# Optimization experiments

Measured on AMD Instinct MI355X. Metric: run time of the kernel, lower is better.

## Reference

```python
import jax, jax.numpy as jnp
import numpy as np

B, S, D_MODEL, N_HEADS, D_FF = 4, 2048, 1024, 16, 4096
HEAD_DIM = D_MODEL // N_HEADS
NUM_BUCKETS, MAX_DISTANCE = 32, 128
EPS = 1e-6


def _relative_position_bucket(relative_position, num_buckets=NUM_BUCKETS, max_distance=MAX_DISTANCE):
    # bidirectional (encoder) variant, matching T5RelativePositionBias
    n = -relative_position
    nb = num_buckets // 2
    ret = (n < 0).astype(jnp.int32) * nb
    n = jnp.abs(n)
    max_exact = nb // 2
    val_if_large = max_exact + (
        jnp.log(jnp.maximum(n, 1).astype(jnp.float32) / max_exact)
        / np.log(max_distance / max_exact) * (nb - max_exact)
    ).astype(jnp.int32)
    val_if_large = jnp.minimum(val_if_large, nb - 1)
    return ret + jnp.where(n < max_exact, n, val_if_large)


def t5_position_bias(rel_emb, q_len, k_len):
    ctx = jnp.arange(q_len)[:, None]
    mem = jnp.arange(k_len)[None, :]
    rp_bucket = _relative_position_bucket(mem - ctx)          # [S, S]
    bias = rel_emb[rp_bucket]                                  # [S, S, H]
    return jnp.transpose(bias, (2, 0, 1))[None]                # [1, H, S, S]


def layer_norm(x, g, b):
    mu = jnp.mean(x, axis=-1, keepdims=True)
    var = jnp.mean(jnp.square(x - mu), axis=-1, keepdims=True)
    return (x - mu) * jax.lax.rsqrt(var + EPS) * g + b


def setup_inputs() -> dict:
    key = jax.random.key(0)
    ks = jax.random.split(key, 20)
    s = 0.02
    p = {
        'src': jax.random.normal(ks[0], (B, S, D_MODEL), jnp.float32),
        'wq': jax.random.normal(ks[1], (D_MODEL, D_MODEL), jnp.float32) * s,
        'bq': jnp.zeros((D_MODEL,), jnp.float32),
        'wk': jax.random.normal(ks[2], (D_MODEL, D_MODEL), jnp.float32) * s,
        'bk': jnp.zeros((D_MODEL,), jnp.float32),
        'wv': jax.random.normal(ks[3], (D_MODEL, D_MODEL), jnp.float32) * s,
        'bv': jnp.zeros((D_MODEL,), jnp.float32),
        'wo': jax.random.normal(ks[4], (D_MODEL, D_MODEL), jnp.float32) * s,
        'bo': jnp.zeros((D_MODEL,), jnp.float32),
        'w1': jax.random.normal(ks[5], (D_MODEL, D_FF), jnp.float32) * s,
        'b1': jnp.zeros((D_FF,), jnp.float32),
        'w2': jax.random.normal(ks[6], (D_FF, D_MODEL), jnp.float32) * s,
        'b2': jnp.zeros((D_MODEL,), jnp.float32),
        'ln1_g': jnp.ones((D_MODEL,), jnp.float32),
        'ln1_b': jnp.zeros((D_MODEL,), jnp.float32),
        'ln2_g': jnp.ones((D_MODEL,), jnp.float32),
        'ln2_b': jnp.zeros((D_MODEL,), jnp.float32),
        'rel_emb': jax.random.normal(ks[7], (NUM_BUCKETS, N_HEADS), jnp.float32) * s,
    }
    return p


def reference(src, wq, bq, wk, bk, wv, bv, wo, bo, w1, b1, w2, b2,
              ln1_g, ln1_b, ln2_g, ln2_b, rel_emb):
    b, s, _ = src.shape

    # --- self-attention block (pre-norm) ---
    xn = layer_norm(src, ln1_g, ln1_b)
    q = (xn @ wq + bq).reshape(b, s, N_HEADS, HEAD_DIM).transpose(0, 2, 1, 3)
    k = (xn @ wk + bk).reshape(b, s, N_HEADS, HEAD_DIM).transpose(0, 2, 1, 3)
    v = (xn @ wv + bv).reshape(b, s, N_HEADS, HEAD_DIM).transpose(0, 2, 1, 3)

    bias = t5_position_bias(rel_emb, s, s)                       # [1,H,S,S]
    scores = jnp.einsum('bhqd,bhkd->bhqk', q, k) / np.sqrt(HEAD_DIM) + bias
    attn = jax.nn.softmax(scores, axis=-1)
    ctx = jnp.einsum('bhqk,bhkd->bhqd', attn, v)                 # [B,H,S,Dh]
    ctx = ctx.transpose(0, 2, 1, 3).reshape(b, s, D_MODEL)
    x = src + (ctx @ wo + bo)

    # --- FFN block (pre-norm, ReLU) ---
    yn = layer_norm(x, ln2_g, ln2_b)
    y = jax.nn.relu(yn @ w1 + b1) @ w2 + b2
    return x + y
```

## Files before the change

### kernel.cpp

```cpp
#include <hip/hip_runtime.h>
#include <math.h>

typedef unsigned short u16;

#define S_LEN 2048
#define BSZ 4
#define DM 1024
#define NH 16
#define HD 64
#define DFF 4096
#define ROWS (BSZ * S_LEN)
#define LOG2E 1.4426950408889634f

typedef __attribute__((__ext_vector_type__(8))) __bf16 bf16x8;
typedef __attribute__((__ext_vector_type__(8))) short short8;
typedef __attribute__((__ext_vector_type__(4))) short short4v;
typedef __attribute__((__ext_vector_type__(4))) float f32x4;
typedef __attribute__((__ext_vector_type__(4))) float float4v;

__device__ __forceinline__ float bf2f(u16 u) {
    union { unsigned int i; float f; } c; c.i = ((unsigned int)u) << 16; return c.f;
}
__device__ __forceinline__ u16 f2bf(float f) {
    union { float f; unsigned int i; } c; c.f = f;
    unsigned int r = c.i + 0x7fffu + ((c.i >> 16) & 1u);
    return (u16)(r >> 16);
}
__device__ __forceinline__ u16 f2bf_cvt(float f) {
    __bf16 h = (__bf16)f;
    return __builtin_bit_cast(u16, h);
}
__device__ __forceinline__ float ldin(const void* p, long i, int f32) {
    return f32 ? ((const float*)p)[i] : bf2f(((const u16*)p)[i]);
}
__device__ __forceinline__ int dtype_f32(const u16* ln1g) {
    return ln1g[0] != 0x3F80;
}
__device__ __forceinline__ void gl_lds16(const void* g, void* l) {
    __builtin_amdgcn_global_load_lds(
        (const __attribute__((address_space(1))) unsigned int*)g,
        (__attribute__((address_space(3))) unsigned int*)l, 16, 0, 0);
}

#define BARR  asm volatile("s_barrier" ::: "memory")
#define LGKM0 asm volatile("s_waitcnt lgkmcnt(0)" ::: "memory")
#define VM4   asm volatile("s_waitcnt vmcnt(4)" ::: "memory")
#define VM0   asm volatile("s_waitcnt vmcnt(0)" ::: "memory")

__device__ __forceinline__ void tr_tile(
    const void* __restrict__ src, u16* __restrict__ dst, int N, int K,
    int bx, int by, int f32, int tid, u16 (*t)[72])
{
#pragma unroll
    for (int i = 0; i < 2; i++) {
        int c = tid + i * 256;
        int row = c >> 3, col = (c & 7) * 8;
        long off = (long)(by * 64 + row) * N + bx * 64 + col;
        short8 v;
        if (f32) {
            const float* s = (const float*)src + off;
            float4v a = *(const float4v*)s;
            float4v b = *(const float4v*)(s + 4);
#pragma unroll
            for (int k = 0; k < 4; k++) { v[k] = (short)f2bf(a[k]); v[k + 4] = (short)f2bf(b[k]); }
        } else {
            v = *(const short8*)((const u16*)src + off);
        }
        *(short8*)(&t[row][col]) = v;
    }
    __syncthreads();
#pragma unroll
    for (int i = 0; i < 2; i++) {
        int c = tid + i * 256;
        int row = c >> 3, col = (c & 7) * 8;
        short8 v;
#pragma unroll
        for (int jj = 0; jj < 8; jj++) v[jj] = (short)t[col + jj][row];
        *(short8*)(dst + (long)(bx * 64 + row) * K + by * 64 + col) = v;
    }
}

__global__ __launch_bounds__(256) void transpose4(
    const void* wq, const void* wk, const void* wv, const void* wo,
    u16* __restrict__ wqkvt, u16* __restrict__ wot, const u16* __restrict__ ln1g)
{
    __shared__ u16 t[64][72];
    int z = blockIdx.z;
    const void* src = (z == 0) ? wq : (z == 1) ? wk : (z == 2) ? wv : wo;
    u16* dst = (z < 3) ? wqkvt + (long)z * 1024 * 1024 : wot;
    tr_tile(src, dst, DM, DM, blockIdx.x, blockIdx.y, dtype_f32(ln1g), threadIdx.x, t);
}

__global__ __launch_bounds__(256) void transpose2(
    const void* w1, const void* w2, u16* __restrict__ w1t, u16* __restrict__ w2t,
    const u16* __restrict__ ln1g)
{
    __shared__ u16 t[64][72];
    int f32 = dtype_f32(ln1g);
    if (blockIdx.z == 0)
        tr_tile(w1, w1t, DFF, DM, blockIdx.x, blockIdx.y, f32, threadIdx.x, t);
    else
        tr_tile(w2, w2t, DM, DFF, blockIdx.y, blockIdx.x, f32, threadIdx.x, t);
}

__global__ __launch_bounds__(256) void vtrans(
    const u16* __restrict__ v, u16* __restrict__ vt)
{
    __shared__ u16 t[64][72];
    int s0 = blockIdx.x * 64;
    int bh = blockIdx.y;
    const u16* src = v + (long)bh * S_LEN * HD;
    u16* dst = vt + (long)bh * HD * S_LEN;
    int tid = threadIdx.x;
#pragma unroll
    for (int i = 0; i < 2; i++) {
        int c = tid + i * 256;
        int row = c >> 3, col = (c & 7) * 8;
        *(short8*)(&t[row][col]) = *(const short8*)(src + (long)(s0 + row) * HD + col);
    }
    __syncthreads();
#pragma unroll
    for (int i = 0; i < 2; i++) {
        int c = tid + i * 256;
        int row = c >> 3, col = (c & 7) * 8;
        short8 o;
#pragma unroll
        for (int jj = 0; jj < 8; jj++) o[jj] = (short)t[col + jj][row];
        *(short8*)(dst + (long)row * S_LEN + s0 + col) = o;
    }
}

__global__ __launch_bounds__(256) void prep_kernel(
    const void* bq, const void* bk, const void* bv, const void* bo,
    const void* b1, const void* b2, const void* l1g, const void* l1b,
    const void* l2g, const void* l2b, const void* rel,
    u16* __restrict__ smalls, float* __restrict__ bias_full)
{
    int f32 = dtype_f32((const u16*)l1g);
    int tid = blockIdx.x * blockDim.x + threadIdx.x;
    if (tid < 13312) {
        float v;
        if      (tid < 1024)  v = ldin(bq,  tid,         f32);
        else if (tid < 2048)  v = ldin(bk,  tid - 1024,  f32);
        else if (tid < 3072)  v = ldin(bv,  tid - 2048,  f32);
        else if (tid < 4096)  v = ldin(bo,  tid - 3072,  f32);
        else if (tid < 8192)  v = ldin(b1,  tid - 4096,  f32);
        else if (tid < 9216)  v = ldin(b2,  tid - 8192,  f32);
        else if (tid < 10240) v = ldin(l1g, tid - 9216,  f32);
        else if (tid < 11264) v = ldin(l1b, tid - 10240, f32);
        else if (tid < 12288) v = ldin(l2g, tid - 11264, f32);
        else                  v = ldin(l2b, tid - 12288, f32);
        smalls[tid] = f2bf(v);
    }
    if (tid < 4095 * 16) {
        int dIdx = tid >> 4;
        int h = tid & 15;
        int delta = dIdx - 2047;
        int n = -delta;
        int ret = (n < 0) ? 16 : 0;
        int na = (n < 0) ? -n : n;
        int bkt;
        if (na < 8) {
            bkt = na;
        } else {
            float tval = logf((float)na * 0.125f) * 2.8853900817779268f;
            int v = 8 + (int)tval;
            bkt = v < 15 ? v : 15;
        }
        bkt += ret;
        bias_full[h * 4095 + dIdx] = ldin(rel, bkt * 16 + h, f32) * LOG2E;
    }
}

__global__ __launch_bounds__(256) void ln_kernel(
    const void* __restrict__ xin, int external, const u16* __restrict__ ln1g,
    const u16* __restrict__ g, const u16* __restrict__ bta, u16* __restrict__ out)
{
    int f32 = external ? dtype_f32(ln1g) : 0;
    int row = blockIdx.x;
    int tid = threadIdx.x;
    float vals[4];
    if (f32) {
        float4v v = *(const float4v*)((const float*)xin + (long)row * DM + tid * 4);
#pragma unroll
        for (int k = 0; k < 4; k++) vals[k] = v[k];
    } else {
        short4v v = *(const short4v*)((const u16*)xin + (long)row * DM + tid * 4);
#pragma unroll
        for (int k = 0; k < 4; k++) vals[k] = bf2f((u16)v[k]);
    }
    float s1 = 0.f, s2 = 0.f;
#pragma unroll
    for (int k = 0; k < 4; k++) { s1 += vals[k]; s2 += vals[k] * vals[k]; }
#pragma unroll
    for (int off = 32; off > 0; off >>= 1) {
        s1 += __shfl_xor(s1, off);
        s2 += __shfl_xor(s2, off);
    }
    __shared__ float ps1[4], ps2[4];
    int wave = tid >> 6, lane = tid & 63;
    if (lane == 0) { ps1[wave] = s1; ps2[wave] = s2; }
    __syncthreads();
    s1 = ps1[0] + ps1[1] + ps1[2] + ps1[3];
    s2 = ps2[0] + ps2[1] + ps2[2] + ps2[3];
    float mu = s1 * (1.0f / DM);
    float var = s2 * (1.0f / DM) - mu * mu;
    float rs = rsqrtf(var + 1e-6f);
    short4v ov;
#pragma unroll
    for (int k = 0; k < 4; k++) {
        float gv = bf2f(g[tid * 4 + k]);
        float bv = bf2f(bta[tid * 4 + k]);
        ov[k] = (short)f2bf((vals[k] - mu) * rs * gv + bv);
    }
    *(short4v*)(out + (long)row * DM + tid * 4) = ov;
}

#define BM 128
#define BN 128
#define BK 64

__global__ __launch_bounds__(256, 3) void gemm_bt(
    const u16* __restrict__ A, const u16* __restrict__ Bt,
    const u16* __restrict__ bias, int M, int N, int K, int mode,
    u16* __restrict__ out_q, u16* __restrict__ out_k, u16* __restrict__ out_v,
    const void* __restrict__ res, void* __restrict__ outp,
    const u16* __restrict__ ln1g)
{
    __shared__ u16 As[BM][BK];
    __shared__ u16 Bs[BN][BK];
    int tid = threadIdx.x;
    int wave = tid >> 6, lane = tid & 63;
    int quad = lane >> 4, l16 = lane & 15;
    int wr = (wave >> 1) * 64, wc = (wave & 1) * 64;

    int nwg = gridDim.x * gridDim.y;
    int bid = blockIdx.y * gridDim.x + blockIdx.x;
    int chunk = nwg >> 3;
    int swz = (bid & 7) * chunk + (bid >> 3);
    int bx = swz % gridDim.x, by = swz / gridDim.x;

    long m0 = (long)by * BM, n0 = (long)bx * BN;
    int flg = (mode == 2 || mode == 4) ? dtype_f32(ln1g) : 0;

    int prow = tid >> 3;
    int pchk = tid & 7;
    int cchk = pchk ^ (prow & 7);
    int skc = cchk * 8;
    int pkc = pchk * 8;
    int rxor = l16 & 7;

    f32x4 acc[4][4];
    f32x4 z = {0.f, 0.f, 0.f, 0.f};
#pragma unroll
    for (int i = 0; i < 4; i++)
#pragma unroll
        for (int j = 0; j < 4; j++) acc[i][j] = z;

    for (int k0 = 0; k0 < K; k0 += BK) {
        __syncthreads();
#pragma unroll
        for (int ro = 0; ro < 4; ro++) {
            gl_lds16(A  + (m0 + ro * 32 + prow) * K + k0 + skc, &As[ro * 32 + prow][pkc]);
            gl_lds16(Bt + (n0 + ro * 32 + prow) * K + k0 + skc, &Bs[ro * 32 + prow][pkc]);
        }
        __syncthreads();
#pragma unroll
        for (int t = 0; t < 2; t++) {
            int rc = ((t * 4 + quad) ^ rxor) * 8;
            bf16x8 af[4], bfr[4];
#pragma unroll
            for (int i = 0; i < 4; i++)
                af[i] = __builtin_bit_cast(bf16x8, *(const short8*)(&As[wr + i * 16 + l16][rc]));
#pragma unroll
            for (int j = 0; j < 4; j++)
                bfr[j] = __builtin_bit_cast(bf16x8, *(const short8*)(&Bs[wc + j * 16 + l16][rc]));
#pragma unroll
            for (int i = 0; i < 4; i++)
#pragma unroll
                for (int j = 0; j < 4; j++)
                    acc[i][j] = __builtin_amdgcn_mfma_f32_16x16x32_bf16(af[i], bfr[j], acc[i][j], 0, 0, 0);
        }
    }

#pragma unroll
    for (int i = 0; i < 4; i++) {
#pragma unroll
        for (int j = 0; j < 4; j++) {
#pragma unroll
            for (int r = 0; r < 4; r++) {
                long gr = m0 + wr + i * 16 + quad * 4 + r;
                long gc = n0 + wc + j * 16 + l16;
                float val = acc[i][j][r] + bf2f(bias[gc]);
                if (mode == 1) {
                    int sel = (int)(gc >> 10);
                    int cc = (int)(gc & 1023);
                    int h = cc >> 6, d = cc & 63;
                    int b = (int)(gr >> 11), s = (int)(gr & 2047);
                    u16* dst = (sel == 0) ? out_q : (sel == 1 ? out_k : out_v);
                    dst[(((long)(b * NH + h)) * S_LEN + s) * HD + d] = f2bf(val);
                } else if (mode == 2) {
                    long idx = gr * N + gc;
                    float rv = flg ? ((const float*)res)[idx]
                                   : bf2f(((const u16*)res)[idx]);
                    ((u16*)outp)[idx] = f2bf(val + rv);
                } else if (mode == 3) {
                    ((u16*)outp)[gr * N + gc] = f2bf(val > 0.f ? val : 0.f);
                } else {
                    long idx = gr * N + gc;
                    float o = val + bf2f(((const u16*)res)[idx]);
                    if (flg) ((float*)outp)[idx] = o;
                    else     ((u16*)outp)[idx]  = f2bf(o);
                }
            }
        }
    }
}

#define TM 256
#define TN 256
#define TK 64

#define PHASE(bi, q, STAGE, WAITV)                                             \
    {                                                                          \
        if ((q) == 0) {                                                        \
            _Pragma("unroll")                                                  \
            for (int j = 0; j < 4; j++) {                                      \
                _Pragma("unroll")                                              \
                for (int t = 0; t < 2; t++)                                    \
                    bfr[j][t] = __builtin_bit_cast(bf16x8, *(const short8*)(   \
                        &Bs[bi][wn * 64 + j * 16 + l16][((t * 4 + quad) ^ rxor) * 8])); \
            }                                                                  \
        }                                                                      \
        _Pragma("unroll")                                                      \
        for (int i = 0; i < 2; i++) {                                          \
            _Pragma("unroll")                                                  \
            for (int t = 0; t < 2; t++)                                        \
                af[i][t] = __builtin_bit_cast(bf16x8, *(const short8*)(        \
                    &As[bi][wm * 128 + ((q) * 2 + i) * 16 + l16][((t * 4 + quad) ^ rxor) * 8])); \
        }                                                                      \
        STAGE                                                                  \
        WAITV;                                                                 \
        BARR;                                                                  \
        LGKM0;                                                                 \
        __builtin_amdgcn_sched_barrier(0);                                     \
        __builtin_amdgcn_s_setprio(1);                                         \
        _Pragma("unroll")                                                      \
        for (int i = 0; i < 2; i++) {                                          \
            _Pragma("unroll")                                                  \
            for (int j = 0; j < 4; j++) {                                      \
                acc[(q) * 2 + i][j] = __builtin_amdgcn_mfma_f32_16x16x32_bf16( \
                    af[i][0], bfr[j][0], acc[(q) * 2 + i][j], 0, 0, 0);        \
                acc[(q) * 2 + i][j] = __builtin_amdgcn_mfma_f32_16x16x32_bf16( \
                    af[i][1], bfr[j][1], acc[(q) * 2 + i][j], 0, 0, 0);        \
            }                                                                  \
        }                                                                      \
        __builtin_amdgcn_s_setprio(0);                                         \
        BARR;                                                                  \
    }

__global__ __launch_bounds__(512, 2) void gemm256(
    const u16* __restrict__ A, const u16* __restrict__ Bt,
    const u16* __restrict__ bias, int M, int N, int K, int mode,
    u16* __restrict__ out_q, u16* __restrict__ out_k, u16* __restrict__ out_v,
    u16* __restrict__ outp)
{
    __shared__ u16 As[2][TM][TK];
    __shared__ u16 Bs[2][TN][TK];

    int tid = threadIdx.x;
    int wavei = tid >> 6, lane = tid & 63;
    int quad = lane >> 4, l16 = lane & 15;
    int wm = wavei >> 2, wn = wavei & 3;

    int nwg = gridDim.x * gridDim.y;
    int bid = blockIdx.y * gridDim.x + blockIdx.x;
    int chunk = nwg >> 3;
    int swz = (bid & 7) * chunk + (bid >> 3);
    int bx = swz % gridDim.x, by = swz / gridDim.x;
    long m0 = (long)by * TM, n0 = (long)bx * TN;

    int srow = tid >> 3;
    int pchk = tid & 7;
    int cchk = pchk ^ (srow & 7);
    int rxor = l16 & 7;

    int NT = K / TK;

    auto stageA = [&](int bufi, int h, int t) {
        const u16* g = A + (m0 + h * 128 + srow) * (long)K + (long)t * TK + cchk * 8;
        gl_lds16(g,                 &As[bufi][h * 128 + srow     ][pchk * 8]);
        gl_lds16(g + 64 * (long)K,  &As[bufi][h * 128 + srow + 64][pchk * 8]);
    };
    auto stageB = [&](int bufi, int h, int t) {
        const u16* g = Bt + (n0 + h * 128 + srow) * (long)K + (long)t * TK + cchk * 8;
        gl_lds16(g,                 &Bs[bufi][h * 128 + srow     ][pchk * 8]);
        gl_lds16(g + 64 * (long)K,  &Bs[bufi][h * 128 + srow + 64][pchk * 8]);
    };

    f32x4 acc[8][4];
    f32x4 z = {0.f, 0.f, 0.f, 0.f};
#pragma unroll
    for (int i = 0; i < 8; i++)
#pragma unroll
        for (int j = 0; j < 4; j++) acc[i][j] = z;

    bf16x8 bfr[4][2];
    bf16x8 af[2][2];

    stageA(0, 0, 0); stageA(0, 1, 0); stageB(0, 0, 0); stageB(0, 1, 0);
    stageB(1, 0, 1); stageB(1, 1, 1);
    VM4;
    BARR;

    for (int kt = 0; kt < NT - 2; kt += 2) {
        PHASE(0, 0, { stageA(1, 0, kt + 1); stageA(1, 1, kt + 1); }, (void)0);
        PHASE(0, 1, { stageB(0, 0, kt + 2); }, (void)0);
        PHASE(0, 2, { stageB(0, 1, kt + 2); }, (void)0);
        PHASE(0, 3, {}, VM4);
        PHASE(1, 0, { stageA(0, 0, kt + 2); }, (void)0);
        PHASE(1, 1, { stageA(0, 1, kt + 2); stageB(1, 0, kt + 3); }, (void)0);
        PHASE(1, 2, { stageB(1, 1, kt + 3); }, (void)0);
        PHASE(1, 3, {}, VM4);
    }
    PHASE(0, 0, { stageA(1, 0, NT - 1); stageA(1, 1, NT - 1); }, (void)0);
    PHASE(0, 1, {}, (void)0);
    PHASE(0, 2, {}, (void)0);
    PHASE(0, 3, {}, VM0);
    PHASE(1, 0, {}, (void)0);
    PHASE(1, 1, {}, (void)0);
    PHASE(1, 2, {}, (void)0);
    PHASE(1, 3, {}, (void)0);

#pragma unroll
    for (int i = 0; i < 8; i++) {
#pragma unroll
        for (int j = 0; j < 4; j++) {
#pragma unroll
            for (int r = 0; r < 4; r++) {
                long gr = m0 + wm * 128 + i * 16 + quad * 4 + r;
                long gc = n0 + wn * 64 + j * 16 + l16;
                float val = acc[i][j][r] + bf2f(bias[gc]);
                if (mode == 1) {
                    int sel = (int)(gc >> 10);
                    int cc = (int)(gc & 1023);
                    int h = cc >> 6, d = cc & 63;
                    int b = (int)(gr >> 11), s = (int)(gr & 2047);
                    u16* dst = (sel == 0) ? out_q : (sel == 1 ? out_k : out_v);
                    dst[(((long)(b * NH + h)) * S_LEN + s) * HD + d] = f2bf(val);
                } else {
                    outp[gr * (long)N + gc] = f2bf(val > 0.f ? val : 0.f);
                }
            }
        }
    }
}

__global__ __launch_bounds__(256, 4) void attn_kernel(
    const u16* __restrict__ Qg, const u16* __restrict__ Kg, const u16* __restrict__ Vtg,
    const float* __restrict__ bias_full, u16* __restrict__ ctx)
{
    __shared__ u16 Ks[64][64];
    __shared__ u16 Vt[64][64];
    __shared__ u16 Ps[64][72];
    __shared__ u16 bias_s[2112];

    int bh = blockIdx.y;
    int b = bh >> 4, h = bh & 15;
    int q0 = blockIdx.x * 64;
    const u16* Q  = Qg  + (long)bh * S_LEN * HD;
    const u16* Kp = Kg  + (long)bh * S_LEN * HD;
    const u16* Vp = Vtg + (long)bh * HD * S_LEN;

    int tid = threadIdx.x;
    int wave = tid >> 6, lane = tid & 63;
    int quad = lane >> 4, l16 = lane & 15;

    for (int i = tid; i < 2112; i += 256)
        bias_s[i] = f2bf(bias_full[h * 4095 + 1984 + i - q0]);
    float Bneg = bias_full[h * 4095 + 0];
    float Bpos = bias_full[h * 4095 + 4094];

    int prow = tid >> 3, pchk = tid & 7;
    int cchk = pchk ^ (prow & 7);
    int rxor = l16 & 7;
    int rc0 = (quad ^ rxor) * 8;
    int rc1 = ((4 + quad) ^ rxor) * 8;

    bf16x8 aq[2];
#pragma unroll
    for (int t = 0; t < 2; t++)
        aq[t] = __builtin_bit_cast(bf16x8,
            *(const short8*)(Q + (long)(q0 + wave * 16 + l16) * HD + t * 32 + quad * 8));

    bf16x8 ones;
#pragma unroll
    for (int i = 0; i < 8; i++) ones[i] = (__bf16)1.0f;

    f32x4 o[4];
    f32x4 z = {0.f, 0.f, 0.f, 0.f};
#pragma unroll
    for (int j = 0; j < 4; j++) o[j] = z;
    f32x4 lacc = z;

    int ib = 63 + quad * 4 - wave * 16 - l16;
    const float c0 = 0.125f * LOG2E;

    for (int t0 = 0; t0 < S_LEN; t0 += 64) {
        __syncthreads();
#pragma unroll
        for (int ro = 0; ro < 2; ro++) {
            gl_lds16(Kp + (long)(t0 + ro * 32 + prow) * HD + cchk * 8,
                     &Ks[ro * 32 + prow][pchk * 8]);
            gl_lds16(Vp + (long)(ro * 32 + prow) * S_LEN + t0 + cchk * 8,
                     &Vt[ro * 32 + prow][pchk * 8]);
        }
        __syncthreads();

        f32x4 s_[4];
#pragma unroll
        for (int j = 0; j < 4; j++) {
            f32x4 a = z;
            bf16x8 kf0 = __builtin_bit_cast(bf16x8, *(const short8*)(&Ks[j * 16 + l16][rc0]));
            a = __builtin_amdgcn_mfma_f32_16x16x32_bf16(kf0, aq[0], a, 0, 0, 0);
            bf16x8 kf1 = __builtin_bit_cast(bf16x8, *(const short8*)(&Ks[j * 16 + l16][rc1]));
            a = __builtin_amdgcn_mfma_f32_16x16x32_bf16(kf1, aq[1], a, 0, 0, 0);
            s_[j] = a;
        }
        int d0 = t0 - q0;
        int nearb = (d0 >= -153 && d0 <= 153);
        float bconst = (d0 > 0) ? Bpos : Bneg;
#pragma unroll
        for (int j = 0; j < 4; j++) {
            short4v pk;
#pragma unroll
            for (int r = 0; r < 4; r++) {
                float bl = nearb ? bf2f(bias_s[ib + t0 + j * 16 + r]) : bconst;
                float p = __builtin_amdgcn_exp2f(fminf(fmaf(s_[j][r], c0, bl), 100.0f));
                pk[r] = (short)f2bf_cvt(p);
            }
            *(short4v*)(&Ps[wave * 16 + l16][j * 16 + quad * 4]) = pk;
        }

        bf16x8 ap[2];
#pragma unroll
        for (int tt = 0; tt < 2; tt++)
            ap[tt] = __builtin_bit_cast(bf16x8,
                *(const short8*)(&Ps[wave * 16 + l16][tt * 32 + quad * 8]));
        lacc = __builtin_amdgcn_mfma_f32_16x16x32_bf16(ap[0], ones, lacc, 0, 0, 0);
        lacc = __builtin_amdgcn_mfma_f32_16x16x32_bf16(ap[1], ones, lacc, 0, 0, 0);
#pragma unroll
        for (int j = 0; j < 4; j++) {
            f32x4 t = o[j];
            bf16x8 bv0 = __builtin_bit_cast(bf16x8, *(const short8*)(&Vt[j * 16 + l16][rc0]));
            t = __builtin_amdgcn_mfma_f32_16x16x32_bf16(ap[0], bv0, t, 0, 0, 0);
            bf16x8 bv1 = __builtin_bit_cast(bf16x8, *(const short8*)(&Vt[j * 16 + l16][rc1]));
            t = __builtin_amdgcn_mfma_f32_16x16x32_bf16(ap[1], bv1, t, 0, 0, 0);
            o[j] = t;
        }
    }

#pragma unroll
    for (int r = 0; r < 4; r++) {
        int qr = wave * 16 + quad * 4 + r;
        float linv = 1.0f / lacc[r];
        long srow = (long)(b * S_LEN + q0 + qr);
#pragma unroll
        for (int j = 0; j < 4; j++)
            ctx[srow * DM + h * HD + j * 16 + l16] = f2bf(o[j][r] * linv);
    }
}

extern "C" void kernel_launch(void* const* d_in, const int* in_sizes, int n_in,
                              void* d_out, int out_size, void* d_ws, size_t ws_size,
                              hipStream_t stream)
{
    const void* src  = d_in[0];
    const void* wq   = d_in[1];
    const void* bq   = d_in[2];
    const void* wk   = d_in[3];
    const void* bk   = d_in[4];
    const void* wv   = d_in[5];
    const void* bv   = d_in[6];
    const void* wo   = d_in[7];
    const void* bo   = d_in[8];
    const void* w1   = d_in[9];
    const void* b1   = d_in[10];
    const void* w2   = d_in[11];
    const void* b2   = d_in[12];
    const void* ln1g = d_in[13];
    const void* ln1b = d_in[14];
    const void* ln2g = d_in[15];
    const void* ln2b = d_in[16];
    const void* rel  = d_in[17];
    const u16* l1g16 = (const u16*)ln1g;

    char* ws = (char*)d_ws;
    const long MB = 1L << 20;
    u16*   smalls = (u16*)  (ws);
    float* bfull  = (float*)(ws + 65536);
    u16*   xn     = (u16*)  (ws + 1  * MB);
    u16*   vtg    = (u16*)  (ws + 1  * MB);
    u16*   qws    = (u16*)  (ws + 17 * MB);
    u16*   kws    = (u16*)  (ws + 33 * MB);
    u16*   vws    = (u16*)  (ws + 49 * MB);
    u16*   hbuf   = (u16*)  (ws + 1  * MB);
    u16*   ctx    = (u16*)  (ws + 65 * MB);
    u16*   yn     = (u16*)  (ws + 65 * MB);
    u16*   xbf    = (u16*)  (ws + 81 * MB);
    u16*   wqkvt  = (u16*)  (ws + 97 * MB);
    u16*   wot    = (u16*)  (ws + 103 * MB);
    u16*   w1t    = (u16*)  (ws + 97 * MB);
    u16*   w2t    = (u16*)  (ws + 105 * MB);

    transpose4<<<dim3(16, 16, 4), 256, 0, stream>>>(wq, wk, wv, wo, wqkvt, wot, l1g16);
    prep_kernel<<<256, 256, 0, stream>>>(bq, bk, bv, bo, b1, b2,
                                         ln1g, ln1b, ln2g, ln2b, rel,
                                         smalls, bfull);

    ln_kernel<<<ROWS, 256, 0, stream>>>(src, 1, l1g16,
                                        smalls + 9216, smalls + 10240, xn);

    gemm256<<<dim3(3072 / TN, ROWS / TM), 512, 0, stream>>>(
        xn, wqkvt, smalls + 0, ROWS, 3072, DM, 1, qws, kws, vws, nullptr);

    vtrans<<<dim3(S_LEN / 64, BSZ * NH), 256, 0, stream>>>(vws, vtg);

    attn_kernel<<<dim3(S_LEN / 64, BSZ * NH), 256, 0, stream>>>(qws, kws, vtg, bfull, ctx);

    gemm_bt<<<dim3(DM / BN, ROWS / BM), 256, 0, stream>>>(
        ctx, wot, smalls + 3072, ROWS, DM, DM, 2,
        nullptr, nullptr, nullptr, src, xbf, l1g16);

    transpose2<<<dim3(64, 16, 2), 256, 0, stream>>>(w1, w2, w1t, w2t, l1g16);

    ln_kernel<<<ROWS, 256, 0, stream>>>(xbf, 0, l1g16,
                                        smalls + 11264, smalls + 12288, yn);

    gemm256<<<dim3(DFF / TN, ROWS / TM), 512, 0, stream>>>(
        yn, w1t, smalls + 4096, ROWS, DFF, DM, 3, nullptr, nullptr, nullptr, hbuf);

    gemm_bt<<<dim3(DM / BN, ROWS / BM), 256, 0, stream>>>(
        hbuf, w2t, smalls + 8192, ROWS, DM, DFF, 4,
        nullptr, nullptr, nullptr, xbf, d_out, l1g16);
}
```

Baseline: 586.3 us.

## Replace output-projection and FFN2 GEMMs with pipelined 256x128 kernel; prefetch K/V in attention

Replaces the simple 128x128 single-buffered gemm_bt with a new 512-thread 256x128 double-buffered GEMM. It uses phased LDS loads, staged global-to-LDS copies with partial vmcnt waits and setprio around the MFMA blocks, and serves the Wo and W2 projections. The attention kernel now register-prefetches the next K/V tile while computing the current one, instead of syncing around each direct global-to-LDS load. It also drops the fminf clamp before exp2. This targets memory latency stalls in the GEMMs and attention, at the cost of more registers and lower occupancy in the new GEMM. Removing the clamp risks overflow if scores are large.

```diff
diff --git a/kernel.cpp b/kernel.cpp
--- a/kernel.cpp
+++ b/kernel.cpp
@@ -45,6 +45,7 @@
 #define BARR  asm volatile("s_barrier" ::: "memory")
 #define LGKM0 asm volatile("s_waitcnt lgkmcnt(0)" ::: "memory")
 #define VM4   asm volatile("s_waitcnt vmcnt(4)" ::: "memory")
+#define VM2   asm volatile("s_waitcnt vmcnt(2)" ::: "memory")
 #define VM0   asm volatile("s_waitcnt vmcnt(0)" ::: "memory")
 
 __device__ __forceinline__ void tr_tile(
@@ -214,107 +215,6 @@
         ov[k] = (short)f2bf((vals[k] - mu) * rs * gv + bv);
     }
     *(short4v*)(out + (long)row * DM + tid * 4) = ov;
-}
-
-#define BM 128
-#define BN 128
-#define BK 64
-
-__global__ __launch_bounds__(256, 3) void gemm_bt(
-    const u16* __restrict__ A, const u16* __restrict__ Bt,
-    const u16* __restrict__ bias, int M, int N, int K, int mode,
-    u16* __restrict__ out_q, u16* __restrict__ out_k, u16* __restrict__ out_v,
-    const void* __restrict__ res, void* __restrict__ outp,
-    const u16* __restrict__ ln1g)
-{
-    __shared__ u16 As[BM][BK];
-    __shared__ u16 Bs[BN][BK];
-    int tid = threadIdx.x;
-    int wave = tid >> 6, lane = tid & 63;
-    int quad = lane >> 4, l16 = lane & 15;
-    int wr = (wave >> 1) * 64, wc = (wave & 1) * 64;
-
-    int nwg = gridDim.x * gridDim.y;
-    int bid = blockIdx.y * gridDim.x + blockIdx.x;
-    int chunk = nwg >> 3;
-    int swz = (bid & 7) * chunk + (bid >> 3);
-    int bx = swz % gridDim.x, by = swz / gridDim.x;
-
-    long m0 = (long)by * BM, n0 = (long)bx * BN;
-    int flg = (mode == 2 || mode == 4) ? dtype_f32(ln1g) : 0;
-
-    int prow = tid >> 3;
-    int pchk = tid & 7;
-    int cchk = pchk ^ (prow & 7);
-    int skc = cchk * 8;
-    int pkc = pchk * 8;
-    int rxor = l16 & 7;
-
-    f32x4 acc[4][4];
-    f32x4 z = {0.f, 0.f, 0.f, 0.f};
-#pragma unroll
-    for (int i = 0; i < 4; i++)
-#pragma unroll
-        for (int j = 0; j < 4; j++) acc[i][j] = z;
-
-    for (int k0 = 0; k0 < K; k0 += BK) {
-        __syncthreads();
-#pragma unroll
-        for (int ro = 0; ro < 4; ro++) {
-            gl_lds16(A  + (m0 + ro * 32 + prow) * K + k0 + skc, &As[ro * 32 + prow][pkc]);
-            gl_lds16(Bt + (n0 + ro * 32 + prow) * K + k0 + skc, &Bs[ro * 32 + prow][pkc]);
-        }
-        __syncthreads();
-#pragma unroll
-        for (int t = 0; t < 2; t++) {
-            int rc = ((t * 4 + quad) ^ rxor) * 8;
-            bf16x8 af[4], bfr[4];
-#pragma unroll
-            for (int i = 0; i < 4; i++)
-                af[i] = __builtin_bit_cast(bf16x8, *(const short8*)(&As[wr + i * 16 + l16][rc]));
-#pragma unroll
-            for (int j = 0; j < 4; j++)
-                bfr[j] = __builtin_bit_cast(bf16x8, *(const short8*)(&Bs[wc + j * 16 + l16][rc]));
-#pragma unroll
-            for (int i = 0; i < 4; i++)
-#pragma unroll
-                for (int j = 0; j < 4; j++)
-                    acc[i][j] = __builtin_amdgcn_mfma_f32_16x16x32_bf16(af[i], bfr[j], acc[i][j], 0, 0, 0);
-        }
-    }
-
-#pragma unroll
-    for (int i = 0; i < 4; i++) {
-#pragma unroll
-        for (int j = 0; j < 4; j++) {
-#pragma unroll
-            for (int r = 0; r < 4; r++) {
-                long gr = m0 + wr + i * 16 + quad * 4 + r;
-                long gc = n0 + wc + j * 16 + l16;
-                float val = acc[i][j][r] + bf2f(bias[gc]);
-                if (mode == 1) {
-                    int sel = (int)(gc >> 10);
-                    int cc = (int)(gc & 1023);
-                    int h = cc >> 6, d = cc & 63;
-                    int b = (int)(gr >> 11), s = (int)(gr & 2047);
-                    u16* dst = (sel == 0) ? out_q : (sel == 1 ? out_k : out_v);
-                    dst[(((long)(b * NH + h)) * S_LEN + s) * HD + d] = f2bf(val);
-                } else if (mode == 2) {
-                    long idx = gr * N + gc;
-                    float rv = flg ? ((const float*)res)[idx]
-                                   : bf2f(((const u16*)res)[idx]);
-                    ((u16*)outp)[idx] = f2bf(val + rv);
-                } else if (mode == 3) {
-                    ((u16*)outp)[gr * N + gc] = f2bf(val > 0.f ? val : 0.f);
-                } else {
-                    long idx = gr * N + gc;
-                    float o = val + bf2f(((const u16*)res)[idx]);
-                    if (flg) ((float*)outp)[idx] = o;
-                    else     ((u16*)outp)[idx]  = f2bf(o);
-                }
-            }
-        }
-    }
 }
 
 #define TM 256
@@ -456,6 +356,145 @@
     }
 }
 
+#define NBM 256
+#define NBN 128
+
+#define PHN(bi, q, STAGE, WAITV)                                               \
+    {                                                                          \
+        if ((q) == 0) {                                                        \
+            _Pragma("unroll")                                                  \
+            for (int j = 0; j < 2; j++) {                                      \
+                _Pragma("unroll")                                              \
+                for (int t = 0; t < 2; t++)                                    \
+                    nbfr[j][t] = __builtin_bit_cast(bf16x8, *(const short8*)(  \
+                        &Bs[bi][wn * 32 + j * 16 + l16][((t * 4 + quad) ^ rxor) * 8])); \
+            }                                                                  \
+        }                                                                      \
+        _Pragma("unroll")                                                      \
+        for (int i = 0; i < 2; i++) {                                          \
+            _Pragma("unroll")                                                  \
+            for (int t = 0; t < 2; t++)                                        \
+                naf[i][t] = __builtin_bit_cast(bf16x8, *(const short8*)(       \
+                    &As[bi][wm * 128 + ((q) * 2 + i) * 16 + l16][((t * 4 + quad) ^ rxor) * 8])); \
+        }                                                                      \
+        STAGE                                                                  \
+        WAITV;                                                                 \
+        BARR;                                                                  \
+        LGKM0;                                                                 \
+        __builtin_amdgcn_sched_barrier(0);                                     \
+        __builtin_amdgcn_s_setprio(1);                                         \
+        _Pragma("unroll")                                                      \
+        for (int i = 0; i < 2; i++) {                                          \
+            _Pragma("unroll")                                                  \
+            for (int j = 0; j < 2; j++) {                                      \
+                acc[(q) * 2 + i][j] = __builtin_amdgcn_mfma_f32_16x16x32_bf16( \
+                    naf[i][0], nbfr[j][0], acc[(q) * 2 + i][j], 0, 0, 0);      \
+                acc[(q) * 2 + i][j] = __builtin_amdgcn_mfma_f32_16x16x32_bf16( \
+                    naf[i][1], nbfr[j][1], acc[(q) * 2 + i][j], 0, 0, 0);      \
+            }                                                                  \
+        }                                                                      \
+        __builtin_amdgcn_s_setprio(0);                                         \
+        BARR;                                                                  \
+    }
+
+__global__ __launch_bounds__(512, 2) void gemm256n(
+    const u16* __restrict__ A, const u16* __restrict__ Bt,
+    const u16* __restrict__ bias, int M, int N, int K, int mode,
+    const void* __restrict__ res, void* __restrict__ outp,
+    const u16* __restrict__ ln1g)
+{
+    __shared__ u16 As[2][NBM][TK];
+    __shared__ u16 Bs[2][NBN][TK];
+
+    int tid = threadIdx.x;
+    int wavei = tid >> 6, lane = tid & 63;
+    int quad = lane >> 4, l16 = lane & 15;
+    int wm = wavei >> 2, wn = wavei & 3;
+
+    int nwg = gridDim.x * gridDim.y;
+    int bid = blockIdx.y * gridDim.x + blockIdx.x;
+    int chunk = nwg >> 3;
+    int swz = (bid & 7) * chunk + (bid >> 3);
+    int bx = swz % gridDim.x, by = swz / gridDim.x;
+    long m0 = (long)by * NBM, n0 = (long)bx * NBN;
+    int flg = dtype_f32(ln1g);
+
+    int srow = tid >> 3;
+    int pchk = tid & 7;
+    int cchk = pchk ^ (srow & 7);
+    int rxor = l16 & 7;
+
+    int NT = K / TK;
+
+    auto stageA = [&](int bufi, int h, int t) {
+        const u16* g = A + (m0 + h * 128 + srow) * (long)K + (long)t * TK + cchk * 8;
+        gl_lds16(g,                 &As[bufi][h * 128 + srow     ][pchk * 8]);
+        gl_lds16(g + 64 * (long)K,  &As[bufi][h * 128 + srow + 64][pchk * 8]);
+    };
+    auto stageB = [&](int bufi, int t) {
+        const u16* g = Bt + (n0 + srow) * (long)K + (long)t * TK + cchk * 8;
+        gl_lds16(g,                 &Bs[bufi][srow     ][pchk * 8]);
+        gl_lds16(g + 64 * (long)K,  &Bs[bufi][srow + 64][pchk * 8]);
+    };
+
+    f32x4 acc[8][2];
+    f32x4 z = {0.f, 0.f, 0.f, 0.f};
+#pragma unroll
+    for (int i = 0; i < 8; i++)
+#pragma unroll
+        for (int j = 0; j < 2; j++) acc[i][j] = z;
+
+    bf16x8 nbfr[2][2];
+    bf16x8 naf[2][2];
+
+    stageA(0, 0, 0); stageA(0, 1, 0); stageB(0, 0);
+    stageB(1, 1);
+    VM2;
+    BARR;
+
+    for (int kt = 0; kt < NT - 2; kt += 2) {
+        PHN(0, 0, { stageA(1, 0, kt + 1); stageA(1, 1, kt + 1); }, (void)0);
+        PHN(0, 1, { stageB(0, kt + 2); }, (void)0);
+        PHN(0, 2, {}, (void)0);
+        PHN(0, 3, {}, VM2);
+        PHN(1, 0, { stageA(0, 0, kt + 2); }, (void)0);
+        PHN(1, 1, { stageA(0, 1, kt + 2); }, (void)0);
+        PHN(1, 2, { stageB(1, kt + 3); }, (void)0);
+        PHN(1, 3, {}, VM2);
+    }
+    PHN(0, 0, { stageA(1, 0, NT - 1); stageA(1, 1, NT - 1); }, (void)0);
+    PHN(0, 1, {}, (void)0);
+    PHN(0, 2, {}, (void)0);
+    PHN(0, 3, {}, VM0);
+    PHN(1, 0, {}, (void)0);
+    PHN(1, 1, {}, (void)0);
+    PHN(1, 2, {}, (void)0);
+    PHN(1, 3, {}, (void)0);
+
+#pragma unroll
+    for (int i = 0; i < 8; i++) {
+#pragma unroll
+        for (int j = 0; j < 2; j++) {
+#pragma unroll
+            for (int r = 0; r < 4; r++) {
+                long gr = m0 + wm * 128 + i * 16 + quad * 4 + r;
+                long gc = n0 + wn * 32 + j * 16 + l16;
+                float val = acc[i][j][r] + bf2f(bias[gc]);
+                long idx = gr * (long)N + gc;
+                if (mode == 2) {
+                    float rv = flg ? ((const float*)res)[idx]
+                                   : bf2f(((const u16*)res)[idx]);
+                    ((u16*)outp)[idx] = f2bf(val + rv);
+                } else {
+                    float o = val + bf2f(((const u16*)res)[idx]);
+                    if (flg) ((float*)outp)[idx] = o;
+                    else     ((u16*)outp)[idx]  = f2bf(o);
+                }
+            }
+        }
+    }
+}
+
 __global__ __launch_bounds__(256, 4) void attn_kernel(
     const u16* __restrict__ Qg, const u16* __restrict__ Kg, const u16* __restrict__ Vtg,
     const float* __restrict__ bias_full, u16* __restrict__ ctx)
@@ -506,17 +545,7 @@
     int ib = 63 + quad * 4 - wave * 16 - l16;
     const float c0 = 0.125f * LOG2E;
 
-    for (int t0 = 0; t0 < S_LEN; t0 += 64) {
-        __syncthreads();
-#pragma unroll
-        for (int ro = 0; ro < 2; ro++) {
-            gl_lds16(Kp + (long)(t0 + ro * 32 + prow) * HD + cchk * 8,
-                     &Ks[ro * 32 + prow][pchk * 8]);
-            gl_lds16(Vp + (long)(ro * 32 + prow) * S_LEN + t0 + cchk * 8,
-                     &Vt[ro * 32 + prow][pchk * 8]);
-        }
-        __syncthreads();
-
+    auto compute = [&](int t0) {
         f32x4 s_[4];
 #pragma unroll
         for (int j = 0; j < 4; j++) {
@@ -536,12 +565,11 @@
 #pragma unroll
             for (int r = 0; r < 4; r++) {
                 float bl = nearb ? bf2f(bias_s[ib + t0 + j * 16 + r]) : bconst;
-                float p = __builtin_amdgcn_exp2f(fminf(fmaf(s_[j][r], c0, bl), 100.0f));
+                float p = __builtin_amdgcn_exp2f(fmaf(s_[j][r], c0, bl));
                 pk[r] = (short)f2bf_cvt(p);
             }
             *(short4v*)(&Ps[wave * 16 + l16][j * 16 + quad * 4]) = pk;
         }
-
         bf16x8 ap[2];
 #pragma unroll
         for (int tt = 0; tt < 2; tt++)
@@ -558,16 +586,56 @@
             t = __builtin_amdgcn_mfma_f32_16x16x32_bf16(ap[1], bv1, t, 0, 0, 0);
             o[j] = t;
         }
+    };
+
+    short8 ka0, ka1, va0, va1, kb0, kb1, vb0, vb1;
+    ka0 = *(const short8*)(Kp + (long)(prow) * HD + cchk * 8);
+    ka1 = *(const short8*)(Kp + (long)(32 + prow) * HD + cchk * 8);
+    va0 = *(const short8*)(Vp + (long)(prow) * S_LEN + cchk * 8);
+    va1 = *(const short8*)(Vp + (long)(32 + prow) * S_LEN + cchk * 8);
+
+    for (int t0 = 0; t0 < S_LEN; t0 += 128) {
+        if (t0 > 0) BARR;
+        VM0;
+        *(short8*)(&Ks[prow][pchk * 8])      = ka0;
+        *(short8*)(&Ks[32 + prow][pchk * 8]) = ka1;
+        *(short8*)(&Vt[prow][pchk * 8])      = va0;
+        *(short8*)(&Vt[32 + prow][pchk * 8]) = va1;
+        {
+            int t1 = t0 + 64;
+            kb0 = *(const short8*)(Kp + (long)(t1 + prow) * HD + cchk * 8);
+            kb1 = *(const short8*)(Kp + (long)(t1 + 32 + prow) * HD + cchk * 8);
+            vb0 = *(const short8*)(Vp + (long)(prow) * S_LEN + t1 + cchk * 8);
+            vb1 = *(const short8*)(Vp + (long)(32 + prow) * S_LEN + t1 + cchk * 8);
+        }
+        LGKM0; BARR;
+        compute(t0);
+
+        BARR;
+        VM0;
+        *(short8*)(&Ks[prow][pchk * 8])      = kb0;
+        *(short8*)(&Ks[32 + prow][pchk * 8]) = kb1;
+        *(short8*)(&Vt[prow][pchk * 8])      = vb0;
+        *(short8*)(&Vt[32 + prow][pchk * 8]) = vb1;
+        if (t0 + 128 < S_LEN) {
+            int t2 = t0 + 128;
+            ka0 = *(const short8*)(Kp + (long)(t2 + prow) * HD + cchk * 8);
+            ka1 = *(const short8*)(Kp + (long)(t2 + 32 + prow) * HD + cchk * 8);
+            va0 = *(const short8*)(Vp + (long)(prow) * S_LEN + t2 + cchk * 8);
+            va1 = *(const short8*)(Vp + (long)(32 + prow) * S_LEN + t2 + cchk * 8);
+        }
+        LGKM0; BARR;
+        compute(t0 + 64);
     }
 
 #pragma unroll
     for (int r = 0; r < 4; r++) {
         int qr = wave * 16 + quad * 4 + r;
         float linv = 1.0f / lacc[r];
-        long srow = (long)(b * S_LEN + q0 + qr);
+        long srow2 = (long)(b * S_LEN + q0 + qr);
 #pragma unroll
         for (int j = 0; j < 4; j++)
-            ctx[srow * DM + h * HD + j * 16 + l16] = f2bf(o[j][r] * linv);
+            ctx[srow2 * DM + h * HD + j * 16 + l16] = f2bf(o[j][r] * linv);
     }
 }
 
@@ -628,9 +696,8 @@
 
     attn_kernel<<<dim3(S_LEN / 64, BSZ * NH), 256, 0, stream>>>(qws, kws, vtg, bfull, ctx);
 
-    gemm_bt<<<dim3(DM / BN, ROWS / BM), 256, 0, stream>>>(
-        ctx, wot, smalls + 3072, ROWS, DM, DM, 2,
-        nullptr, nullptr, nullptr, src, xbf, l1g16);
+    gemm256n<<<dim3(DM / NBN, ROWS / NBM), 512, 0, stream>>>(
+        ctx, wot, smalls + 3072, ROWS, DM, DM, 2, src, xbf, l1g16);
 
     transpose2<<<dim3(64, 16, 2), 256, 0, stream>>>(w1, w2, w1t, w2t, l1g16);
 
@@ -640,7 +707,6 @@
     gemm256<<<dim3(DFF / TN, ROWS / TM), 512, 0, stream>>>(
         yn, w1t, smalls + 4096, ROWS, DFF, DM, 3, nullptr, nullptr, nullptr, hbuf);
 
-    gemm_bt<<<dim3(DM / BN, ROWS / BM), 256, 0, stream>>>(
-        hbuf, w2t, smalls + 8192, ROWS, DM, DFF, 4,
-        nullptr, nullptr, nullptr, xbf, d_out, l1g16);
-}
+    gemm256n<<<dim3(DM / NBN, ROWS / NBM), 512, 0, stream>>>(
+        hbuf, w2t, smalls + 8192, ROWS, DM, DFF, 4, xbf, d_out, l1g16);
+}
```

After: 588.2 us. No clear change (+0.3%).
